# Kernel tuning notes

Measured on AMD Instinct MI355X. Metric: run time of the kernel, lower is better.

## Reference

```python
import jax, jax.numpy as jnp
import numpy as np

N = 50000      # nodes
E = 800000     # edges
D = 128        # h_dim
R = 8          # num_rel
B = 4          # num_bases (< R -> basis decomposition)
L = 2          # num_conv
BN_EPS = 1e-3  # keras BatchNormalization default epsilon


def setup_inputs() -> dict:
    key = jax.random.key(0)
    ks = jax.random.split(key, 10)
    node_feat = jax.random.normal(ks[0], (N, D), dtype=jnp.float32)
    src = jax.random.randint(ks[1], (E,), 0, N)
    dst = jax.random.randint(ks[2], (E,), 0, N)
    etype = jax.random.randint(ks[3], (E,), 0, R)
    s = 1.0 / np.sqrt(D)
    W_emb = jax.random.normal(ks[4], (D, D), dtype=jnp.float32) * s
    b_emb = jnp.zeros((D,), dtype=jnp.float32)
    bases = jax.random.normal(ks[5], (L, B, D, D), dtype=jnp.float32) * s
    w_coe = jax.random.normal(ks[6], (L, R, B), dtype=jnp.float32) * 0.3
    self_loop = jax.random.normal(ks[7], (L, D, D), dtype=jnp.float32) * s
    bn_gamma = jnp.ones((L, D), dtype=jnp.float32)
    bn_beta = jnp.zeros((L, D), dtype=jnp.float32)
    bn_mean = jnp.zeros((L, D), dtype=jnp.float32)
    bn_var = jnp.ones((L, D), dtype=jnp.float32)
    return {"node_feat": node_feat, "W_emb": W_emb, "b_emb": b_emb,
            "bases": bases, "w_coe": w_coe, "self_loop": self_loop,
            "bn_gamma": bn_gamma, "bn_beta": bn_beta,
            "bn_mean": bn_mean, "bn_var": bn_var,
            "src": src, "dst": dst, "etype": etype}


def _edge_norm(etype, dst, dtype):
    # compute_norm: per edge type r, node_norm[dst] = 1/(#edges of type r into dst),
    # later types overwrite earlier ones (tensor_scatter_nd_update in the loop).
    node_norm = jnp.zeros((N,), dtype=dtype)
    for r in range(R):  # unique edge types, fixed ascending order
        mask = (etype == r).astype(dtype)
        cnt = jax.ops.segment_sum(mask, dst, num_segments=N)
        node_norm = jnp.where(cnt > 0, 1.0 / jnp.maximum(cnt, 1.0), node_norm)
    return node_norm[dst][:, None]  # [E, 1], norm of each edge's destination


def reference(node_feat, W_emb, b_emb, bases, w_coe, self_loop,
              bn_gamma, bn_beta, bn_mean, bn_var, src, dst, etype):
    # embedding Dense
    h = node_feat @ W_emb + b_emb                     # [N, D]
    norm = _edge_norm(etype, dst, h.dtype)            # [E, 1]
    for l in range(L):
        # basis decomposition: W[r] = sum_b w_coe[r,b] * bases[b]
        W = jnp.einsum('rb,bdf->rdf', w_coe[l], bases[l])   # [R, D, D]
        # transform all nodes under every relation, then gather per edge
        # (same math as per-type boolean_mask + matmul in low_mem path)
        T = jnp.einsum('nd,rdf->rnf', h, W)                 # [R, N, D]
        msg = T[etype, src] * norm                          # [E, D]
        agg = jax.ops.segment_sum(msg, dst, num_segments=N) # sum reduce -> [N, D]
        h = agg + h @ self_loop[l]
        # BatchNormalization, inference mode (training=None)
        h = bn_gamma[l] * (h - bn_mean[l]) * jax.lax.rsqrt(bn_var[l] + BN_EPS) + bn_beta[l]
        h = jax.nn.relu(h)
        # Dropout is identity at inference
    return h
```

## Files before the change

### kernel.cpp

```cpp
#include <hip/hip_runtime.h>

#define Dh 128
#define NN 50000
#define EE 800000
#define RR 8
#define BB 4
#define LL 2
#define KTOT 640
#define KA0 512
#define BN_EPS 1e-3f
#define NR (NN * RR)
#define NBLK 196

#define N8    (NN * Dh / 8)
#define BT_N  (LL * Dh * KTOT)
#define WE_N  (Dh * Dh)
#define EPI_N (3 * Dh)
#define Z4_N  (NR / 4)
#define PREP_TOT (N8 + BT_N + WE_N + EPI_N + Z4_N)

typedef __attribute__((ext_vector_type(8))) short bf16x8;
typedef __attribute__((ext_vector_type(4))) float f32x4;
typedef __attribute__((ext_vector_type(2))) float f32x2;

__device__ inline unsigned short f2bf(float x) {
    unsigned u = __float_as_uint(x);
    unsigned r = (u + 0x7fffu + ((u >> 16) & 1u)) >> 16;
    return (unsigned short)r;
}

__global__ __launch_bounds__(256) void prep_kernel(
    const float* __restrict__ nf, const float* __restrict__ bases,
    const float* __restrict__ self_loop, const float* __restrict__ W_emb,
    const float* __restrict__ b_emb,
    const float* __restrict__ bn_gamma, const float* __restrict__ bn_beta,
    const float* __restrict__ bn_mean, const float* __restrict__ bn_var,
    unsigned short* __restrict__ nf_bf, unsigned short* __restrict__ BT,
    unsigned short* __restrict__ WembT,
    float* __restrict__ sc, float* __restrict__ sh, int* __restrict__ counts)
{
    int idx = blockIdx.x * 256 + threadIdx.x;
    if (idx < N8) {
        size_t base = (size_t)idx * 8;
        float4 v0 = *(const float4*)&nf[base];
        float4 v1 = *(const float4*)&nf[base + 4];
        unsigned short o[8] = { f2bf(v0.x), f2bf(v0.y), f2bf(v0.z), f2bf(v0.w),
                                f2bf(v1.x), f2bf(v1.y), f2bf(v1.z), f2bf(v1.w) };
        *(uint4*)&nf_bf[base] = *(uint4*)o;
        return;
    }
    idx -= N8;
    if (idx < BT_N) {
        int l = idx / (Dh * KTOT);
        int rem = idx - l * (Dh * KTOT);
        int f = rem / KTOT;
        int k = rem - f * KTOT;
        float v;
        if (k < KA0) v = bases[(((l * BB + (k >> 7)) * Dh) + (k & 127)) * Dh + f];
        else         v = self_loop[((size_t)l * Dh + (k - KA0)) * Dh + f];
        BT[(size_t)(l * Dh + f) * KTOT + k] = f2bf(v);
        return;
    }
    idx -= BT_N;
    if (idx < WE_N) {
        int f = idx >> 7, d = idx & 127;
        WembT[f * Dh + d] = f2bf(W_emb[d * Dh + f]);
        return;
    }
    idx -= WE_N;
    if (idx < EPI_N) {
        int cfg = idx >> 7, d = idx & 127;
        float s, t;
        if (cfg == 0) { s = 1.f; t = b_emb[d]; }
        else {
            int l = cfg - 1;
            float sv = bn_gamma[l * Dh + d] * rsqrtf(bn_var[l * Dh + d] + BN_EPS);
            s = sv;
            t = bn_beta[l * Dh + d] - bn_mean[l * Dh + d] * sv;
        }
        sc[cfg * Dh + d] = s; sh[cfg * Dh + d] = t;
        return;
    }
    idx -= EPI_N;
    if (idx < Z4_N) ((int4*)counts)[idx] = make_int4(0, 0, 0, 0);
}

__global__ __launch_bounds__(256) void gemm_bn_kernel(
    const unsigned short* __restrict__ A0, int ka0,
    const unsigned short* __restrict__ A1,
    const unsigned short* __restrict__ BT, int K,
    const float* __restrict__ sc, const float* __restrict__ sh,
    void* __restrict__ outp, int out_fp32, int do_relu, int M)
{
    __shared__ unsigned short a_s[64][72];
    __shared__ unsigned short b_s[128][72];
    int t = threadIdx.x;
    int wave = t >> 6, lane = t & 63;
    int n16 = lane & 15, quad = lane >> 4;
    int row0 = blockIdx.x * 64;

    f32x4 acc[8];
    #pragma unroll
    for (int j = 0; j < 8; j++) acc[j] = (f32x4){0.f, 0.f, 0.f, 0.f};

    int nchunk = K >> 6;
    for (int ch = 0; ch < nchunk; ch++) {
        int k0 = ch * 64;
        {
            int srow = t >> 2, seg = t & 3;
            int gr = row0 + srow;
            int kk = k0 + seg * 16;
            const uint4* gp;
            if (kk < ka0) gp = (const uint4*)&A0[(size_t)gr * ka0 + kk];
            else          gp = (const uint4*)&A1[(size_t)gr * Dh + (kk - ka0)];
            #pragma unroll
            for (int i = 0; i < 2; i++) {
                uint4 v = make_uint4(0u, 0u, 0u, 0u);
                if (gr < M) v = gp[i];
                *(uint4*)&a_s[srow][seg * 16 + i * 8] = v;
            }
        }
        {
            int f = t >> 1, seg = t & 1;
            const uint4* bp = (const uint4*)&BT[(size_t)f * K + k0 + seg * 32];
            #pragma unroll
            for (int i = 0; i < 4; i++)
                *(uint4*)&b_s[f][seg * 32 + i * 8] = bp[i];
        }
        __syncthreads();
        #pragma unroll
        for (int ks = 0; ks < 2; ks++) {
            bf16x8 af, bfr[8];
            af = *(const bf16x8*)&a_s[wave * 16 + n16][ks * 32 + quad * 8];
            #pragma unroll
            for (int j = 0; j < 8; j++)
                bfr[j] = *(const bf16x8*)&b_s[j * 16 + n16][ks * 32 + quad * 8];
            #pragma unroll
            for (int j = 0; j < 8; j++)
                acc[j] = __builtin_amdgcn_mfma_f32_16x16x32_bf16(
                    af, bfr[j], acc[j], 0, 0, 0);
        }
        __syncthreads();
    }

    float sj[8], tj[8];
    #pragma unroll
    for (int j = 0; j < 8; j++) {
        int col = j * 16 + n16;
        sj[j] = sc[col]; tj[j] = sh[col];
    }
    #pragma unroll
    for (int v = 0; v < 4; v++) {
        int gr = row0 + wave * 16 + quad * 4 + v;
        if (gr < M) {
            #pragma unroll
            for (int j = 0; j < 8; j++) {
                float y = acc[j][v] * sj[j] + tj[j];
                if (do_relu) y = fmaxf(y, 0.f);
                int col = j * 16 + n16;
                if (out_fp32) ((float*)outp)[(size_t)gr * Dh + col] = y;
                else ((unsigned short*)outp)[(size_t)gr * Dh + col] = f2bf(y);
            }
        }
    }
}

__global__ __launch_bounds__(256) void count_kernel(
    const int* __restrict__ dst, const int* __restrict__ etype,
    int* __restrict__ counts)
{
    int idx = blockIdx.x * 256 + threadIdx.x;
    if (idx >= EE / 4) return;
    int4 d = ((const int4*)dst)[idx];
    int4 t = ((const int4*)etype)[idx];
    atomicAdd(&counts[d.x * RR + t.x], 1);
    atomicAdd(&counts[d.y * RR + t.y], 1);
    atomicAdd(&counts[d.z * RR + t.z], 1);
    atomicAdd(&counts[d.w * RR + t.w], 1);
}

__global__ __launch_bounds__(256) void norm_scan1_kernel(
    const int* __restrict__ counts, float* __restrict__ node_norm,
    int* __restrict__ row_ptr, int* __restrict__ bsum)
{
    __shared__ int s[256];
    int t = threadIdx.x;
    int n = blockIdx.x * 256 + t;
    int total = 0; float norm = 0.f;
    if (n < NN) {
        #pragma unroll
        for (int r = 0; r < RR; r++) {
            int c = counts[n * RR + r];
            total += c;
            if (c > 0) norm = 1.0f / (float)c;
        }
        node_norm[n] = norm;
    }
    s[t] = total;
    __syncthreads();
    #pragma unroll
    for (int off = 1; off < 256; off <<= 1) {
        int v = (t >= off) ? s[t - off] : 0;
        __syncthreads();
        s[t] += v;
        __syncthreads();
    }
    if (n < NN) row_ptr[n] = s[t] - total;
    if (t == 255) bsum[blockIdx.x] = s[255];
}

__global__ __launch_bounds__(256) void scan2_kernel(
    const int* __restrict__ bsum, int* __restrict__ boffset)
{
    __shared__ int s[256];
    int t = threadIdx.x;
    int d = (t < NBLK) ? bsum[t] : 0;
    s[t] = d;
    __syncthreads();
    #pragma unroll
    for (int off = 1; off < 256; off <<= 1) {
        int v = (t >= off) ? s[t - off] : 0;
        __syncthreads();
        s[t] += v;
        __syncthreads();
    }
    if (t <= NBLK) boffset[t] = s[t] - d;
}

__global__ __launch_bounds__(256) void scan3_kernel(
    int* __restrict__ row_ptr, int* __restrict__ cursor,
    const int* __restrict__ boffset)
{
    int t = threadIdx.x;
    int n = blockIdx.x * 256 + t;
    if (n < NN) {
        int v = row_ptr[n] + boffset[blockIdx.x];
        row_ptr[n] = v;
        cursor[n]  = v;
    }
    if (blockIdx.x == 0 && t == 0) row_ptr[NN] = EE;
}

__global__ __launch_bounds__(256) void fill_kernel(
    const int* __restrict__ src, const int* __restrict__ dst,
    const int* __restrict__ etype, int* __restrict__ cursor,
    unsigned* __restrict__ packed)
{
    int idx = blockIdx.x * 256 + threadIdx.x;
    if (idx >= EE / 4) return;
    int4 d  = ((const int4*)dst)[idx];
    int4 sr = ((const int4*)src)[idx];
    int4 et = ((const int4*)etype)[idx];
    int p0 = atomicAdd(&cursor[d.x], 1);
    int p1 = atomicAdd(&cursor[d.y], 1);
    int p2 = atomicAdd(&cursor[d.z], 1);
    int p3 = atomicAdd(&cursor[d.w], 1);
    packed[p0] = (unsigned)sr.x | ((unsigned)et.x << 16);
    packed[p1] = (unsigned)sr.y | ((unsigned)et.y << 16);
    packed[p2] = (unsigned)sr.z | ((unsigned)et.z << 16);
    packed[p3] = (unsigned)sr.w | ((unsigned)et.w << 16);
}

__global__ __launch_bounds__(256) void agg_basis_kernel(
    const unsigned* __restrict__ h32, const int* __restrict__ row_ptr,
    const unsigned* __restrict__ packed, const float* __restrict__ node_norm,
    const float* __restrict__ wco,
    unsigned* __restrict__ aggB)
{
    __shared__ float4 co_s[RR];
    int t = threadIdx.x;
    if (t < RR) co_s[t] = ((const float4*)wco)[t];
    __syncthreads();
    int wave = t >> 6, lane = t & 63;
    int n = blockIdx.x * 4 + wave;
    if (n >= NN) return;
    int s = row_ptr[n];
    int e = row_ptr[n + 1];
    f32x2 a[BB];
    #pragma unroll
    for (int b = 0; b < BB; b++) a[b] = (f32x2){0.f, 0.f};
    int i = s;
    for (; i + 8 <= e; i += 8) {
        unsigned p[8], hv[8];
        #pragma unroll
        for (int k = 0; k < 8; k++) p[k] = packed[i + k];
        #pragma unroll
        for (int k = 0; k < 8; k++)
            hv[k] = h32[(size_t)(p[k] & 0xffffu) * 64 + lane];
        #pragma unroll
        for (int k = 0; k < 8; k++) {
            float4 co = co_s[p[k] >> 16];
            f32x2 v = (f32x2){ __uint_as_float(hv[k] << 16),
                               __uint_as_float(hv[k] & 0xffff0000u) };
            a[0] += co.x * v;
            a[1] += co.y * v;
            a[2] += co.z * v;
            a[3] += co.w * v;
        }
    }
    if (i < e) {
        unsigned p[8], hv[8];
        #pragma unroll
        for (int k = 0; k < 8; k++) {
            int j = i + k;
            p[k] = packed[j < e ? j : (e - 1)];
        }
        #pragma unroll
        for (int k = 0; k < 8; k++)
            hv[k] = h32[(size_t)(p[k] & 0xffffu) * 64 + lane];
        #pragma unroll
        for (int k = 0; k < 8; k++) {
            float vm = (i + k < e) ? 1.f : 0.f;
            float4 co = co_s[p[k] >> 16];
            f32x2 v = (f32x2){ __uint_as_float(hv[k] << 16) * vm,
                               __uint_as_float(hv[k] & 0xffff0000u) * vm };
            a[0] += co.x * v;
            a[1] += co.y * v;
            a[2] += co.z * v;
            a[3] += co.w * v;
        }
    }
    float norm = node_norm[n];
    #pragma unroll
    for (int b = 0; b < BB; b++) {
        unsigned o = (unsigned)f2bf(a[b].x * norm) |
                     ((unsigned)f2bf(a[b].y * norm) << 16);
        aggB[(size_t)n * 256 + b * 64 + lane] = o;
    }
}

extern "C" void kernel_launch(void* const* d_in, const int* in_sizes, int n_in,
                              void* d_out, int out_size, void* d_ws, size_t ws_size,
                              hipStream_t stream)
{
    const float* node_feat = (const float*)d_in[0];
    const float* W_emb     = (const float*)d_in[1];
    const float* b_emb     = (const float*)d_in[2];
    const float* bases     = (const float*)d_in[3];
    const float* w_coe     = (const float*)d_in[4];
    const float* self_loop = (const float*)d_in[5];
    const float* bn_gamma  = (const float*)d_in[6];
    const float* bn_beta   = (const float*)d_in[7];
    const float* bn_mean   = (const float*)d_in[8];
    const float* bn_var    = (const float*)d_in[9];
    const int*   src       = (const int*)d_in[10];
    const int*   dst       = (const int*)d_in[11];
    const int*   etype     = (const int*)d_in[12];

    char* ws = (char*)d_ws;
    size_t off = 0;
    unsigned short* h0 = (unsigned short*)(ws + off);     off += (size_t)NN * Dh * 2;
    unsigned short* h1 = (unsigned short*)(ws + off);     off += (size_t)NN * Dh * 2;
    unsigned short* nf_bf = (unsigned short*)(ws + off);  off += (size_t)NN * Dh * 2;
    unsigned short* aggB = (unsigned short*)(ws + off);   off += (size_t)NN * KA0 * 2;
    unsigned short* BT = (unsigned short*)(ws + off);     off += (size_t)LL * Dh * KTOT * 2;
    unsigned short* WembT = (unsigned short*)(ws + off);  off += (size_t)Dh * Dh * 2;
    float* sc = (float*)(ws + off);                       off += 3 * Dh * 4;
    float* sh = (float*)(ws + off);                       off += 3 * Dh * 4;
    float* node_norm = (float*)(ws + off);                off += (size_t)NN * 4;
    int* counts = (int*)(ws + off);                       off += (size_t)NR * 4;
    int* row_ptr = (int*)(ws + off);                      off += ((size_t)NN + 4) * 4;
    int* cursor = (int*)(ws + off);                       off += (size_t)NN * 4;
    int* bsum = (int*)(ws + off);                         off += 256 * 4;
    int* boffset = (int*)(ws + off);                      off += 260 * 4;
    unsigned* packed = (unsigned*)(ws + off);             off += (size_t)EE * 4;

    const int e4_blocks = (EE / 4 + 255) / 256;
    const int node_blocks = (NN + 255) / 256;
    const int prep_blocks = (PREP_TOT + 255) / 256;
    const int gemm_blocks = (NN + 63) / 64;
    const int agg_blocks = (NN + 3) / 4;

    prep_kernel<<<prep_blocks, 256, 0, stream>>>(
        node_feat, bases, self_loop, W_emb, b_emb,
        bn_gamma, bn_beta, bn_mean, bn_var,
        nf_bf, BT, WembT, sc, sh, counts);

    count_kernel<<<e4_blocks, 256, 0, stream>>>(dst, etype, counts);
    norm_scan1_kernel<<<node_blocks, 256, 0, stream>>>(counts, node_norm, row_ptr, bsum);
    scan2_kernel<<<1, 256, 0, stream>>>(bsum, boffset);
    scan3_kernel<<<node_blocks, 256, 0, stream>>>(row_ptr, cursor, boffset);
    fill_kernel<<<e4_blocks, 256, 0, stream>>>(src, dst, etype, cursor, packed);

    gemm_bn_kernel<<<gemm_blocks, 256, 0, stream>>>(
        nf_bf, Dh, nullptr, WembT, Dh, sc, sh, h0, 0, 0, NN);

    agg_basis_kernel<<<agg_blocks, 256, 0, stream>>>(
        (const unsigned*)h0, row_ptr, packed, node_norm, w_coe, (unsigned*)aggB);
    gemm_bn_kernel<<<gemm_blocks, 256, 0, stream>>>(
        aggB, KA0, h0, BT, KTOT, sc + Dh, sh + Dh, h1, 0, 1, NN);

    agg_basis_kernel<<<agg_blocks, 256, 0, stream>>>(
        (const unsigned*)h1, row_ptr, packed, node_norm, w_coe + RR * BB, (unsigned*)aggB);
    gemm_bn_kernel<<<gemm_blocks, 256, 0, stream>>>(
        aggB, KA0, h1, BT + Dh * KTOT, KTOT, sc + 2 * Dh, sh + 2 * Dh, d_out, 1, 1, NN);
}
```

Before: 322.5 us.

## Replace fill-phase atomics with per-edge ranks from count pass

The count kernel now keeps the return value of its atomicAdd as a per-edge rank within its (dst, etype) bucket and stores it as a ushort. The scan kernels turn the counts into exclusive per-(node, type) offsets. The fill kernel then computes each edge's slot directly instead of running a second round of atomics on a per-node cursor. This removes one contended atomic pass and groups edges by type within each node, at the cost of an extra 1.6 MB rank array written and read, plus more counts traffic in the scan kernels.

```diff
diff --git a/kernel.cpp b/kernel.cpp
--- a/kernel.cpp
+++ b/kernel.cpp
@@ -167,20 +167,22 @@
 
 __global__ __launch_bounds__(256) void count_kernel(
     const int* __restrict__ dst, const int* __restrict__ etype,
-    int* __restrict__ counts)
+    int* __restrict__ counts, unsigned short* __restrict__ rank)
 {
     int idx = blockIdx.x * 256 + threadIdx.x;
     if (idx >= EE / 4) return;
     int4 d = ((const int4*)dst)[idx];
     int4 t = ((const int4*)etype)[idx];
-    atomicAdd(&counts[d.x * RR + t.x], 1);
-    atomicAdd(&counts[d.y * RR + t.y], 1);
-    atomicAdd(&counts[d.z * RR + t.z], 1);
-    atomicAdd(&counts[d.w * RR + t.w], 1);
+    int r0 = atomicAdd(&counts[d.x * RR + t.x], 1);
+    int r1 = atomicAdd(&counts[d.y * RR + t.y], 1);
+    int r2 = atomicAdd(&counts[d.z * RR + t.z], 1);
+    int r3 = atomicAdd(&counts[d.w * RR + t.w], 1);
+    ((ushort4*)rank)[idx] = make_ushort4((unsigned short)r0, (unsigned short)r1,
+                                         (unsigned short)r2, (unsigned short)r3);
 }
 
 __global__ __launch_bounds__(256) void norm_scan1_kernel(
-    const int* __restrict__ counts, float* __restrict__ node_norm,
+    int* __restrict__ counts, float* __restrict__ node_norm,
     int* __restrict__ row_ptr, int* __restrict__ bsum)
 {
     __shared__ int s[256];
@@ -188,12 +190,16 @@
     int n = blockIdx.x * 256 + t;
     int total = 0; float norm = 0.f;
     if (n < NN) {
+        int pre[RR];
         #pragma unroll
         for (int r = 0; r < RR; r++) {
             int c = counts[n * RR + r];
+            pre[r] = total;
             total += c;
             if (c > 0) norm = 1.0f / (float)c;
         }
+        #pragma unroll
+        for (int r = 0; r < RR; r++) counts[n * RR + r] = pre[r];
         node_norm[n] = norm;
     }
     s[t] = total;
@@ -228,7 +234,7 @@
 }
 
 __global__ __launch_bounds__(256) void scan3_kernel(
-    int* __restrict__ row_ptr, int* __restrict__ cursor,
+    int* __restrict__ row_ptr, int* __restrict__ counts,
     const int* __restrict__ boffset)
 {
     int t = threadIdx.x;
@@ -236,25 +242,27 @@
     if (n < NN) {
         int v = row_ptr[n] + boffset[blockIdx.x];
         row_ptr[n] = v;
-        cursor[n]  = v;
+        #pragma unroll
+        for (int r = 0; r < RR; r++) counts[n * RR + r] += v;
     }
     if (blockIdx.x == 0 && t == 0) row_ptr[NN] = EE;
 }
 
 __global__ __launch_bounds__(256) void fill_kernel(
     const int* __restrict__ src, const int* __restrict__ dst,
-    const int* __restrict__ etype, int* __restrict__ cursor,
-    unsigned* __restrict__ packed)
+    const int* __restrict__ etype, const unsigned short* __restrict__ rank,
+    const int* __restrict__ counts, unsigned* __restrict__ packed)
 {
     int idx = blockIdx.x * 256 + threadIdx.x;
     if (idx >= EE / 4) return;
     int4 d  = ((const int4*)dst)[idx];
     int4 sr = ((const int4*)src)[idx];
     int4 et = ((const int4*)etype)[idx];
-    int p0 = atomicAdd(&cursor[d.x], 1);
-    int p1 = atomicAdd(&cursor[d.y], 1);
-    int p2 = atomicAdd(&cursor[d.z], 1);
-    int p3 = atomicAdd(&cursor[d.w], 1);
+    ushort4 rk = ((const ushort4*)rank)[idx];
+    int p0 = counts[d.x * RR + et.x] + rk.x;
+    int p1 = counts[d.y * RR + et.y] + rk.y;
+    int p2 = counts[d.z * RR + et.z] + rk.z;
+    int p3 = counts[d.w * RR + et.w] + rk.w;
     packed[p0] = (unsigned)sr.x | ((unsigned)et.x << 16);
     packed[p1] = (unsigned)sr.y | ((unsigned)et.y << 16);
     packed[p2] = (unsigned)sr.z | ((unsigned)et.z << 16);
@@ -360,7 +368,7 @@
     float* node_norm = (float*)(ws + off);                off += (size_t)NN * 4;
     int* counts = (int*)(ws + off);                       off += (size_t)NR * 4;
     int* row_ptr = (int*)(ws + off);                      off += ((size_t)NN + 4) * 4;
-    int* cursor = (int*)(ws + off);                       off += (size_t)NN * 4;
+    unsigned short* rank = (unsigned short*)(ws + off);   off += (size_t)EE * 2;
     int* bsum = (int*)(ws + off);                         off += 256 * 4;
     int* boffset = (int*)(ws + off);                      off += 260 * 4;
     unsigned* packed = (unsigned*)(ws + off);             off += (size_t)EE * 4;
@@ -376,11 +384,11 @@
         bn_gamma, bn_beta, bn_mean, bn_var,
         nf_bf, BT, WembT, sc, sh, counts);
 
-    count_kernel<<<e4_blocks, 256, 0, stream>>>(dst, etype, counts);
+    count_kernel<<<e4_blocks, 256, 0, stream>>>(dst, etype, counts, rank);
     norm_scan1_kernel<<<node_blocks, 256, 0, stream>>>(counts, node_norm, row_ptr, bsum);
     scan2_kernel<<<1, 256, 0, stream>>>(bsum, boffset);
-    scan3_kernel<<<node_blocks, 256, 0, stream>>>(row_ptr, cursor, boffset);
-    fill_kernel<<<e4_blocks, 256, 0, stream>>>(src, dst, etype, cursor, packed);
+    scan3_kernel<<<node_blocks, 256, 0, stream>>>(row_ptr, counts, boffset);
+    fill_kernel<<<e4_blocks, 256, 0, stream>>>(src, dst, etype, rank, counts, packed);
 
     gemm_bn_kernel<<<gemm_blocks, 256, 0, stream>>>(
         nf_bf, Dh, nullptr, WembT, Dh, sc, sh, h0, 0, 0, NN);
```

After: 293.5 us. 9.0% less time.
